# Kernel tuning notes

Hardware: AMD Instinct MI355X
Metric: run time of the kernel (lower is better)

## Reference

```python
import jax, jax.numpy as jnp
import numpy as np

D = 2048
N_EXPERTS = 64
K = 2


def setup_inputs() -> dict:
    key = jax.random.key(0)
    kx, kw = jax.random.split(key)
    x = jax.random.normal(kx, (4, 4096, D), dtype=jnp.float32)
    # xavier_uniform for Linear(d, n_experts): bound = sqrt(6/(fan_in+fan_out))
    bound = float(np.sqrt(6.0 / (D + N_EXPERTS)))
    W = jax.random.uniform(kw, (N_EXPERTS, D), dtype=jnp.float32, minval=-bound, maxval=bound)
    b = jnp.zeros((N_EXPERTS,), dtype=jnp.float32)
    return {"x": x, "W": W, "b": b}


def reference(x, W, b):
    # logits: [B, S, E]  (eval mode: no noise)
    logits = jnp.einsum("bsd,ed->bse", x, W) + b
    topk_vals, topk_idx = jax.lax.top_k(logits, K)  # [B, S, K]
    gates = jax.nn.softmax(topk_vals, axis=-1)
    return gates, topk_idx
```

## Files before the change

### kernel.cpp

```cpp
#include <hip/hip_runtime.h>
#include <math.h>

#define DD 2048
#define EE 64
#define TM 64
#define BK 64
#define NCHUNK (DD / BK)
#define THREADS 256
#define LDSTR (TM + 4)

__global__ __launch_bounds__(THREADS) void router_kernel(
    const float* __restrict__ x, const float* __restrict__ W,
    const float* __restrict__ bias_g, float* __restrict__ out, int n_tokens)
{
    __shared__ float xs[BK * LDSTR];
    __shared__ float ws[BK * LDSTR];
    __shared__ float logits[TM * (EE + 1)];

    const int tid = threadIdx.x;
    const int tx  = tid & 15;
    const int ty  = tid >> 4;
    const int tBase = blockIdx.x * TM;

    const float* xg = x + (size_t)tBase * DD;

    float acc[4][4];
#pragma unroll
    for (int i = 0; i < 4; ++i)
#pragma unroll
        for (int j = 0; j < 4; ++j) acc[i][j] = 0.f;

    float bvals[4];
#pragma unroll
    for (int j = 0; j < 4; ++j) bvals[j] = bias_g[tx * 4 + j];

    float4 rx[4], rw[4];

#define LOAD_TILES(k0)                                                        \
    {                                                                         \
        _Pragma("unroll")                                                     \
        for (int p = 0; p < 4; ++p) {                                         \
            rx[p] = *(const float4*)&xg[(size_t)(ty + 16 * p) * DD + (k0) + tx * 4]; \
            rw[p] = *(const float4*)&W [(size_t)(ty + 16 * p) * DD + (k0) + tx * 4]; \
        }                                                                     \
    }

    LOAD_TILES(0);

    for (int c = 0; c < NCHUNK; ++c) {
        __syncthreads();
#pragma unroll
        for (int p = 0; p < 4; ++p) {
            const int col = ty + 16 * p;
            const int kk  = tx * 4;
            xs[(kk + 0) * LDSTR + col] = rx[p].x;
            xs[(kk + 1) * LDSTR + col] = rx[p].y;
            xs[(kk + 2) * LDSTR + col] = rx[p].z;
            xs[(kk + 3) * LDSTR + col] = rx[p].w;
            ws[(kk + 0) * LDSTR + col] = rw[p].x;
            ws[(kk + 1) * LDSTR + col] = rw[p].y;
            ws[(kk + 2) * LDSTR + col] = rw[p].z;
            ws[(kk + 3) * LDSTR + col] = rw[p].w;
        }
        __syncthreads();

        if (c + 1 < NCHUNK) {
            const int k0n = (c + 1) * BK;
            LOAD_TILES(k0n);
        }

#pragma unroll
        for (int k = 0; k < BK; ++k) {
            const float4 xv = *(const float4*)&xs[k * LDSTR + ty * 4];
            const float4 wv = *(const float4*)&ws[k * LDSTR + tx * 4];
            acc[0][0] += xv.x * wv.x; acc[0][1] += xv.x * wv.y;
            acc[0][2] += xv.x * wv.z; acc[0][3] += xv.x * wv.w;
            acc[1][0] += xv.y * wv.x; acc[1][1] += xv.y * wv.y;
            acc[1][2] += xv.y * wv.z; acc[1][3] += xv.y * wv.w;
            acc[2][0] += xv.z * wv.x; acc[2][1] += xv.z * wv.y;
            acc[2][2] += xv.z * wv.z; acc[2][3] += xv.z * wv.w;
            acc[3][0] += xv.w * wv.x; acc[3][1] += xv.w * wv.y;
            acc[3][2] += xv.w * wv.z; acc[3][3] += xv.w * wv.w;
        }
    }

    __syncthreads();
#pragma unroll
    for (int i = 0; i < 4; ++i)
#pragma unroll
        for (int j = 0; j < 4; ++j)
            logits[(ty * 4 + i) * (EE + 1) + (tx * 4 + j)] = acc[i][j] + bvals[j];
    __syncthreads();

    if (tid < TM) {
        const float* lrow = &logits[tid * (EE + 1)];
        float v1 = -INFINITY, v2 = -INFINITY;
        int   i1 = 0, i2 = 0;
        for (int e = 0; e < EE; ++e) {
            const float v = lrow[e];
            if (v > v1) { v2 = v1; i2 = i1; v1 = v; i1 = e; }
            else if (v > v2) { v2 = v; i2 = e; }
        }
        const float ed = expf(v2 - v1);
        const float inv = 1.f / (1.f + ed);
        const int tok = tBase + tid;
        out[tok * 2 + 0] = inv;
        out[tok * 2 + 1] = ed * inv;
        float* oidx = out + (size_t)2 * n_tokens;
        oidx[tok * 2 + 0] = (float)i1;
        oidx[tok * 2 + 1] = (float)i2;
    }
}

extern "C" void kernel_launch(void* const* d_in, const int* in_sizes, int n_in,
                              void* d_out, int out_size, void* d_ws, size_t ws_size,
                              hipStream_t stream) {
    const float* x = (const float*)d_in[0];
    const float* W = (const float*)d_in[1];
    const float* b = (const float*)d_in[2];
    float* out = (float*)d_out;

    const int n_tokens = in_sizes[0] / DD;
    const int n_blocks = n_tokens / TM;

    router_kernel<<<n_blocks, THREADS, 0, stream>>>(x, W, b, out, n_tokens);
}
```

Before: 246.2 us.

## Halve token tile to 32 and redo global load mapping for coalescing

Shrinks the per-block token tile from 64 to 32, which doubles the grid to 512 blocks so more CUs get work. Global loads are remapped so consecutive threads read contiguous float4s along a row (8 or 4 threads per row) instead of 16 threads across rows, with separate LDS strides for x and W. Each thread now computes a 2x4 micro-tile, so the 64x2048 W tile is re-read from L2 by twice as many blocks and there is less arithmetic per LDS load.

```diff
diff --git a/kernel.cpp b/kernel.cpp
--- a/kernel.cpp
+++ b/kernel.cpp
@@ -3,64 +3,74 @@
 
 #define DD 2048
 #define EE 64
-#define TM 64
+#define TM 32
 #define BK 64
 #define NCHUNK (DD / BK)
 #define THREADS 256
-#define LDSTR (TM + 4)
+#define LDSX 34
+#define LDSW 68
 
 __global__ __launch_bounds__(THREADS) void router_kernel(
     const float* __restrict__ x, const float* __restrict__ W,
     const float* __restrict__ bias_g, float* __restrict__ out, int n_tokens)
 {
-    __shared__ float xs[BK * LDSTR];
-    __shared__ float ws[BK * LDSTR];
-    __shared__ float logits[TM * (EE + 1)];
+    __shared__ __attribute__((aligned(16))) float xs[BK * LDSX];
+    __shared__ __attribute__((aligned(16))) float ws[BK * LDSW];
+    __shared__ __attribute__((aligned(16))) float logits[TM * (EE + 1)];
 
     const int tid = threadIdx.x;
     const int tx  = tid & 15;
     const int ty  = tid >> 4;
     const int tBase = blockIdx.x * TM;
 
-    const float* xg = x + (size_t)tBase * DD;
+    const int xt = tid >> 3;
+    const int xc = tid & 7;
+    const int we = tid >> 2;
+    const int wc = tid & 3;
 
-    float acc[4][4];
+    const float* xrow = x + (size_t)(tBase + xt) * DD;
+    const float* wrow = W + (size_t)we * DD;
+
+    float acc[2][4];
 #pragma unroll
-    for (int i = 0; i < 4; ++i)
+    for (int t = 0; t < 2; ++t)
 #pragma unroll
-        for (int j = 0; j < 4; ++j) acc[i][j] = 0.f;
+        for (int j = 0; j < 4; ++j) acc[t][j] = 0.f;
 
-    float bvals[4];
-#pragma unroll
-    for (int j = 0; j < 4; ++j) bvals[j] = bias_g[tx * 4 + j];
+    const float4 bv4 = *(const float4*)&bias_g[tx * 4];
 
-    float4 rx[4], rw[4];
+    float4 rx[2], rw[4];
 
-#define LOAD_TILES(k0)                                                        \
-    {                                                                         \
-        _Pragma("unroll")                                                     \
-        for (int p = 0; p < 4; ++p) {                                         \
-            rx[p] = *(const float4*)&xg[(size_t)(ty + 16 * p) * DD + (k0) + tx * 4]; \
-            rw[p] = *(const float4*)&W [(size_t)(ty + 16 * p) * DD + (k0) + tx * 4]; \
-        }                                                                     \
+#define LOAD_TILES(k0)                                                       \
+    {                                                                        \
+        _Pragma("unroll")                                                    \
+        for (int p = 0; p < 2; ++p)                                          \
+            rx[p] = *(const float4*)&xrow[(k0) + 4 * (xc + 8 * p)];          \
+        _Pragma("unroll")                                                    \
+        for (int p = 0; p < 4; ++p)                                          \
+            rw[p] = *(const float4*)&wrow[(k0) + 4 * (wc + 4 * p)];          \
     }
 
     LOAD_TILES(0);
 
     for (int c = 0; c < NCHUNK; ++c) {
         __syncthreads();
+
+#pragma unroll
+        for (int p = 0; p < 2; ++p) {
+            const int k = 4 * (xc + 8 * p);
+            xs[(k + 0) * LDSX + xt] = rx[p].x;
+            xs[(k + 1) * LDSX + xt] = rx[p].y;
+            xs[(k + 2) * LDSX + xt] = rx[p].z;
+            xs[(k + 3) * LDSX + xt] = rx[p].w;
+        }
 #pragma unroll
         for (int p = 0; p < 4; ++p) {
-            const int col = ty + 16 * p;
-            const int kk  = tx * 4;
-            xs[(kk + 0) * LDSTR + col] = rx[p].x;
-            xs[(kk + 1) * LDSTR + col] = rx[p].y;
-            xs[(kk + 2) * LDSTR + col] = rx[p].z;
-            xs[(kk + 3) * LDSTR + col] = rx[p].w;
-            ws[(kk + 0) * LDSTR + col] = rw[p].x;
-            ws[(kk + 1) * LDSTR + col] = rw[p].y;
-            ws[(kk + 2) * LDSTR + col] = rw[p].z;
-            ws[(kk + 3) * LDSTR + col] = rw[p].w;
+            const int k = 4 * (wc + 4 * p);
+            ws[(k + 0) * LDSW + we] = rw[p].x;
+            ws[(k + 1) * LDSW + we] = rw[p].y;
+            ws[(k + 2) * LDSW + we] = rw[p].z;
+            ws[(k + 3) * LDSW + we] = rw[p].w;
         }
         __syncthreads();
 
@@ -71,25 +81,24 @@
 
 #pragma unroll
         for (int k = 0; k < BK; ++k) {
-            const float4 xv = *(const float4*)&xs[k * LDSTR + ty * 4];
-            const float4 wv = *(const float4*)&ws[k * LDSTR + tx * 4];
+            const float2 xv = *(const float2*)&xs[k * LDSX + ty * 2];
+            const float4 wv = *(const float4*)&ws[k * LDSW + tx * 4];
             acc[0][0] += xv.x * wv.x; acc[0][1] += xv.x * wv.y;
             acc[0][2] += xv.x * wv.z; acc[0][3] += xv.x * wv.w;
             acc[1][0] += xv.y * wv.x; acc[1][1] += xv.y * wv.y;
             acc[1][2] += xv.y * wv.z; acc[1][3] += xv.y * wv.w;
-            acc[2][0] += xv.z * wv.x; acc[2][1] += xv.z * wv.y;
-            acc[2][2] += xv.z * wv.z; acc[2][3] += xv.z * wv.w;
-            acc[3][0] += xv.w * wv.x; acc[3][1] += xv.w * wv.y;
-            acc[3][2] += xv.w * wv.z; acc[3][3] += xv.w * wv.w;
         }
     }
 
     __syncthreads();
 #pragma unroll
-    for (int i = 0; i < 4; ++i)
-#pragma unroll
-        for (int j = 0; j < 4; ++j)
-            logits[(ty * 4 + i) * (EE + 1) + (tx * 4 + j)] = acc[i][j] + bvals[j];
+    for (int t = 0; t < 2; ++t) {
+        const int row = (ty * 2 + t) * (EE + 1);
+        logits[row + tx * 4 + 0] = acc[t][0] + bv4.x;
+        logits[row + tx * 4 + 1] = acc[t][1] + bv4.y;
+        logits[row + tx * 4 + 2] = acc[t][2] + bv4.z;
+        logits[row + tx * 4 + 3] = acc[t][3] + bv4.w;
+    }
     __syncthreads();
 
     if (tid < TM) {
```

After: 235.4 us, median of 2. -4.4%, faster.
